# Kernel optimization log

Hardware: AMD Instinct MI355X
Metric: run time of the kernel (lower is better)

Reference implementation:

```python
import jax, jax.numpy as jnp
import numpy as np

HEADS = 8
DIM_HEAD = 64


def setup_inputs() -> dict:
    key = jax.random.key(0)
    ks = jax.random.split(key, 10)
    B, NQ, NK, D, INNER = 4, 2048, 2048, 1024, HEADS * DIM_HEAD
    w_scale = 0.02
    return {
        "x": jax.random.normal(ks[0], (B, NQ, D), jnp.float32),
        "context": jax.random.normal(ks[1], (B, NK, D), jnp.float32),
        "wq": jax.random.normal(ks[2], (D, INNER), jnp.float32) * w_scale,
        "bq": jax.random.normal(ks[3], (INNER,), jnp.float32) * w_scale,
        "wk": jax.random.normal(ks[4], (D, INNER), jnp.float32) * w_scale,
        "bk": jax.random.normal(ks[5], (INNER,), jnp.float32) * w_scale,
        "wv": jax.random.normal(ks[6], (D, INNER), jnp.float32) * w_scale,
        "bv": jax.random.normal(ks[7], (INNER,), jnp.float32) * w_scale,
        "wo": jax.random.normal(ks[8], (INNER, D), jnp.float32) * w_scale,
        "bo": jax.random.normal(ks[9], (D,), jnp.float32) * w_scale,
    }


def _split_heads(t):
    # [b, n, h*d] -> [b, h, n, d]
    b, n, _ = t.shape
    return t.reshape(b, n, HEADS, DIM_HEAD).transpose(0, 2, 1, 3)


def reference(x, context, wq, bq, wk, bk, wv, bv, wo, bo):
    scale = DIM_HEAD ** -0.5
    q = _split_heads(x @ wq + bq)        # [b, h, nq, d]
    k = _split_heads(context @ wk + bk)  # [b, h, nk, d]
    v = _split_heads(context @ wv + bv)  # [b, h, nk, d]
    sim = jnp.einsum('bhid,bhjd->bhij', q, k) * scale  # full score matrix, as in original
    attn = jax.nn.softmax(sim, axis=-1)
    out = jnp.einsum('bhij,bhjd->bhid', attn, v)       # [b, h, nq, d]
    b, h, n, d = out.shape
    out = out.transpose(0, 2, 1, 3).reshape(b, n, h * d)
    return out @ wo + bo
```

## Files before the change

### kernel.cpp

```cpp
#include <hip/hip_runtime.h>
#include <hip/hip_bf16.h>

typedef __attribute__((ext_vector_type(8))) short short8;
typedef __attribute__((ext_vector_type(4))) float f32x4;
typedef __attribute__((ext_vector_type(2))) unsigned uint2u;

__device__ __forceinline__ short f2bf(float f) {
  union { float f; unsigned u; } x; x.f = f;
  unsigned r = x.u + 0x7fffu + ((x.u >> 16) & 1u);
  return (short)(r >> 16);
}

__device__ __forceinline__ unsigned cvt_pk_bf16(float a, float b) {
  unsigned r;
  asm("v_cvt_pk_bf16_f32 %0, %1, %2" : "=v"(r) : "v"(a), "v"(b));
  return r;
}

__device__ __forceinline__ float fast_exp2(float x) {
#if __has_builtin(__builtin_amdgcn_exp2f)
  return __builtin_amdgcn_exp2f(x);
#else
  return exp2f(x);
#endif
}

__device__ __forceinline__ void gload16(const short* g, short* l) {
  __builtin_amdgcn_global_load_lds(
      (const __attribute__((address_space(1))) unsigned*)g,
      (__attribute__((address_space(3))) unsigned*)l, 16, 0, 0);
}

__device__ __forceinline__ void barrier_lgkm() {
  asm volatile("s_waitcnt lgkmcnt(0)" ::: "memory");
  __builtin_amdgcn_s_barrier();
}

__global__ __launch_bounds__(256) void prep_kernel(
    const float* __restrict__ x, const float* __restrict__ ctx,
    const float* __restrict__ wq, const float* __restrict__ wk,
    const float* __restrict__ wv, const float* __restrict__ wo,
    short* __restrict__ xc, short* __restrict__ wqt, short* __restrict__ wkt,
    short* __restrict__ wvt, short* __restrict__ wot) {
  __shared__ short tile[64][72];
  int bx = blockIdx.x;
  if (bx < 16384) {
    int i = (bx * 256 + threadIdx.x) * 4;
    const float* s = (i < (1 << 23)) ? x : ctx;
    int j = i & ((1 << 23) - 1);
    float4 f = *(const float4*)(s + j);
    union { short s[4]; uint2 u; } o;
    o.s[0] = f2bf(f.x); o.s[1] = f2bf(f.y);
    o.s[2] = f2bf(f.z); o.s[3] = f2bf(f.w);
    *(uint2*)(xc + i) = o.u;
    return;
  }
  int t = bx - 16384;
  int z = t >> 7, bb = t & 127;
  const float* src = (z == 0) ? wq : (z == 1) ? wk : (z == 2) ? wv : wo;
  short* dst = (z == 0) ? wqt : (z == 1) ? wkt : (z == 2) ? wvt : wot;
  int R = (z < 3) ? 1024 : 512, C = (z < 3) ? 512 : 1024;
  int tpc = C >> 6;
  int bxx = bb % tpc, by = bb / tpc;
  int r0 = by * 64, c0 = bxx * 64;
  int tx = threadIdx.x & 15, ty = threadIdx.x >> 4;
#pragma unroll
  for (int i = 0; i < 4; i++) {
    int r = i * 16 + ty;
    float4 f = *(const float4*)(src + (size_t)(r0 + r) * C + c0 + tx * 4);
    union { short s[4]; uint2 u; } o;
    o.s[0] = f2bf(f.x); o.s[1] = f2bf(f.y);
    o.s[2] = f2bf(f.z); o.s[3] = f2bf(f.w);
    *(uint2*)&tile[r][tx * 4] = o.u;
  }
  __syncthreads();
#pragma unroll
  for (int i = 0; i < 4; i++) {
    int c = i * 16 + ty;
    union { short s[4]; uint2 u; } o;
#pragma unroll
    for (int k = 0; k < 4; k++) o.s[k] = tile[tx * 4 + k][c];
    *(uint2*)(dst + (size_t)(c0 + c) * R + r0 + tx * 4) = o.u;
  }
}


template <bool SWAP>
__device__ __forceinline__ void gemm_core_2ph(
    const short* __restrict__ A, const short* __restrict__ Bt, int K,
    int mblk, int nblk, short* sA, short* sB, f32x4 (&acc)[4][4]) {
  int tid = threadIdx.x;
  int lane = tid & 63, wave = tid >> 6;
  int quad = lane >> 4, l15 = lane & 15;
  int wm = (wave >> 1) * 64, wn = (wave & 1) * 64;
  int sub = lane >> 3, e8 = lane & 7;
  int swz = (e8 ^ sub) << 3;
  int s0 = (quad ^ (l15 & 7)) << 3;
  const short* Ag = A + (size_t)(mblk + 32 * wave + sub) * K + swz;
  const short* Bg = Bt + (size_t)(nblk + 32 * wave + sub) * K + swz;
  short* Al = sA + 4 * wave * 512;
  short* Bl = sB + 4 * wave * 512;

  auto STAGE = [&](int b, int k0) {
    short* a = Al + b * 8192;
    short* bb = Bl + b * 8192;
#pragma unroll
    for (int t = 0; t < 4; t++) {
      gload16(Ag + (size_t)(8 * t) * K + k0, a + t * 512);
      gload16(Bg + (size_t)(8 * t) * K + k0, bb + t * 512);
    }
  };

  int nsteps = K >> 6;
  STAGE(0, 0);
  __syncthreads();
  int buf = 0;
  for (int step = 0; step < nsteps; ++step) {
    if (step + 1 < nsteps) STAGE(buf ^ 1, (step + 1) << 6);
    const short* sAb = sA + buf * 8192;
    const short* sBb = sB + buf * 8192;
#pragma unroll
    for (int h = 0; h < 2; h++) {
      int so = s0 ^ (h << 5);
      short8 af[4], bf[4];
#pragma unroll
      for (int mt = 0; mt < 4; mt++)
        af[mt] = *(const short8*)(&sAb[(wm + mt * 16 + l15) * 64 + so]);
#pragma unroll
      for (int nt = 0; nt < 4; nt++)
        bf[nt] = *(const short8*)(&sBb[(wn + nt * 16 + l15) * 64 + so]);
#pragma unroll
      for (int mt = 0; mt < 4; mt++)
#pragma unroll
        for (int nt = 0; nt < 4; nt++) {
          if (SWAP)
            acc[mt][nt] = __builtin_amdgcn_mfma_f32_16x16x32_bf16(
                bf[nt], af[mt], acc[mt][nt], 0, 0, 0);
          else
            acc[mt][nt] = __builtin_amdgcn_mfma_f32_16x16x32_bf16(
                af[mt], bf[nt], acc[mt][nt], 0, 0, 0);
        }
    }
    __syncthreads();
    buf ^= 1;
  }
}

template <bool SWAP>
__device__ __forceinline__ void gemm_core_1buf(
    const short* __restrict__ A, const short* __restrict__ Bt, int K,
    int mblk, int nblk, short* sA, short* sB, f32x4 (&acc)[4][4]) {
  int tid = threadIdx.x;
  int lane = tid & 63, wave = tid >> 6;
  int quad = lane >> 4, l15 = lane & 15;
  int wm = (wave >> 1) * 64, wn = (wave & 1) * 64;
  int sub = lane >> 3, e8 = lane & 7;
  int swz = (e8 ^ sub) << 3;
  int s0 = (quad ^ (l15 & 7)) << 3;
  const short* Ag = A + (size_t)(mblk + 32 * wave + sub) * K + swz;
  const short* Bg = Bt + (size_t)(nblk + 32 * wave + sub) * K + swz;
  short* Al = sA + 4 * wave * 512;
  short* Bl = sB + 4 * wave * 512;

  for (int k0 = 0; k0 < K; k0 += 64) {
    __syncthreads();
#pragma unroll
    for (int t = 0; t < 4; t++) {
      gload16(Ag + (size_t)(8 * t) * K + k0, Al + t * 512);
      gload16(Bg + (size_t)(8 * t) * K + k0, Bl + t * 512);
    }
    __syncthreads();
#pragma unroll
    for (int h = 0; h < 2; h++) {
      int so = s0 ^ (h << 5);
      short8 af[4], bf[4];
#pragma unroll
      for (int mt = 0; mt < 4; mt++)
        af[mt] = *(const short8*)(&sA[(wm + mt * 16 + l15) * 64 + so]);
#pragma unroll
      for (int nt = 0; nt < 4; nt++)
        bf[nt] = *(const short8*)(&sB[(wn + nt * 16 + l15) * 64 + so]);
#pragma unroll
      for (int mt = 0; mt < 4; mt++)
#pragma unroll
        for (int nt = 0; nt < 4; nt++) {
          if (SWAP)
            acc[mt][nt] = __builtin_amdgcn_mfma_f32_16x16x32_bf16(
                bf[nt], af[mt], acc[mt][nt], 0, 0, 0);
          else
            acc[mt][nt] = __builtin_amdgcn_mfma_f32_16x16x32_bf16(
                af[mt], bf[nt], acc[mt][nt], 0, 0, 0);
        }
    }
  }
}

__global__ __launch_bounds__(256) void gemm_qkv(
    const short* __restrict__ xb, const short* __restrict__ cb,
    const short* __restrict__ wqt, const short* __restrict__ wkt,
    const short* __restrict__ wvt,
    const float* __restrict__ bq, const float* __restrict__ bk,
    const float* __restrict__ bv,
    short* __restrict__ Qb, short* __restrict__ Kb, short* __restrict__ Vt) {
  __shared__ __align__(16) short sA[2 * 128 * 64];
  __shared__ __align__(16) short sB[2 * 128 * 64];
  int z = blockIdx.z;
  const short* A  = (z == 0) ? xb : cb;
  const short* Bt = (z == 0) ? wqt : (z == 1) ? wkt : wvt;
  const float* bias = (z == 0) ? bq : (z == 1) ? bk : bv;
  short* out = (z == 0) ? Qb : (z == 1) ? Kb : Vt;
  float scale = (z == 0) ? 0.18033688011112042f : 1.0f;
  int mblk = blockIdx.x * 128, nblk = blockIdx.y * 128;
  int lane = threadIdx.x & 63, wave = threadIdx.x >> 6;
  int quad = lane >> 4, l15 = lane & 15;
  int wm = (wave >> 1) * 64, wn = (wave & 1) * 64;

  if (z == 2) {
    f32x4 acc[4][4] = {};
    gemm_core_2ph<false>(A, Bt, 1024, mblk, nblk, sA, sB, acc);
#pragma unroll
    for (int nt = 0; nt < 4; nt++) {
      int col = nblk + wn + nt * 16 + l15;
      float bias_v = bias[col];
      int h = col >> 6, dh = col & 63;
#pragma unroll
      for (int mt = 0; mt < 4; mt++) {
        int row0 = mblk + wm + mt * 16 + quad * 4;
        int b = row0 >> 11, n0 = row0 & 2047;
        size_t base = ((size_t)(b * 8 + h)) << 17;
        union { short s[4]; uint2 u; } pk;
#pragma unroll
        for (int r = 0; r < 4; r++) pk.s[r] = f2bf(acc[mt][nt][r] + bias_v);
        *(uint2*)(out + base + ((size_t)dh << 11) + n0) = pk.u;
      }
    }
  } else {
    f32x4 acc[4][4] = {};
    gemm_core_2ph<true>(A, Bt, 1024, mblk, nblk, sA, sB, acc);
#pragma unroll
    for (int nt = 0; nt < 4; nt++) {
      int colbase = nblk + wn + nt * 16 + quad * 4;
      float4 b4 = *(const float4*)(bias + colbase);
      int h = colbase >> 6, dh0 = colbase & 63;
#pragma unroll
      for (int mt = 0; mt < 4; mt++) {
        int row = mblk + wm + mt * 16 + l15;
        int b = row >> 11, n = row & 2047;
        size_t base = ((size_t)(b * 8 + h)) << 17;
        union { short s[4]; uint2 u; } pk;
        pk.s[0] = f2bf((acc[mt][nt][0] + b4.x) * scale);
        pk.s[1] = f2bf((acc[mt][nt][1] + b4.y) * scale);
        pk.s[2] = f2bf((acc[mt][nt][2] + b4.z) * scale);
        pk.s[3] = f2bf((acc[mt][nt][3] + b4.w) * scale);
        *(uint2*)(out + base + ((size_t)n << 6) + dh0) = pk.u;
      }
    }
  }
}

__global__ __launch_bounds__(256) void gemm_out(
    const short* __restrict__ Ob, const short* __restrict__ wot,
    const float* __restrict__ bo, float* __restrict__ out) {
  __shared__ __align__(16) short sA[128 * 64];
  __shared__ __align__(16) short sB[128 * 64];
  int mblk = blockIdx.x * 128, nblk = blockIdx.y * 128;
  f32x4 acc[4][4] = {};
  gemm_core_1buf<true>(Ob, wot, 512, mblk, nblk, sA, sB, acc);
  int lane = threadIdx.x & 63, wave = threadIdx.x >> 6;
  int quad = lane >> 4, l15 = lane & 15;
  int wm = (wave >> 1) * 64, wn = (wave & 1) * 64;
#pragma unroll
  for (int nt = 0; nt < 4; nt++) {
    int colbase = nblk + wn + nt * 16 + quad * 4;
    float4 b4 = *(const float4*)(bo + colbase);
#pragma unroll
    for (int mt = 0; mt < 4; mt++) {
      int row = mblk + wm + mt * 16 + l15;
      f32x4 v;
      v[0] = acc[mt][nt][0] + b4.x; v[1] = acc[mt][nt][1] + b4.y;
      v[2] = acc[mt][nt][2] + b4.z; v[3] = acc[mt][nt][3] + b4.w;
      *(f32x4*)(out + (size_t)row * 1024 + colbase) = v;
    }
  }
}

__global__ __launch_bounds__(256, 2) void attn_kernel(
    const short* __restrict__ Qb, const short* __restrict__ Kb,
    const short* __restrict__ Vt, short* __restrict__ Ob) {
  __shared__ __align__(16) short sK[2 * 64 * 64];
  __shared__ __align__(16) short sV[2 * 64 * 64];
  int tid = threadIdx.x;
  int lane = tid & 63, wave = tid >> 6;
  int quad = lane >> 4, l15 = lane & 15;
  int bh = blockIdx.x & 31;
  int qt = blockIdx.x >> 5;
  const short* Qp = Qb + ((size_t)bh << 17);
  const short* Kp = Kb + ((size_t)bh << 17);
  const short* Vp = Vt + ((size_t)bh << 17);
  int qrow0 = qt * 128 + wave * 32;

  short8 qf[2][2];
#pragma unroll
  for (int g = 0; g < 2; g++) {
    const short* qrow = Qp + (size_t)(qrow0 + g * 16 + l15) * 64;
    qf[g][0] = *(const short8*)(qrow + quad * 8);
    qf[g][1] = *(const short8*)(qrow + 32 + quad * 8);
  }

  int jk0 = 2 * wave, jk1 = 2 * wave + 1;
  int sub = lane >> 3;
  int e8  = lane & 7;
  int swz = (e8 ^ sub) << 3;
  const short* kg0 = Kp + (size_t)(8 * jk0 + sub) * 64 + e8 * 8;
  const short* kg1 = Kp + (size_t)(8 * jk1 + sub) * 64 + e8 * 8;
  const short* vg0 = Vp + (size_t)(8 * jk0 + sub) * 2048 + e8 * 8;
  const short* vg1 = Vp + (size_t)(8 * jk1 + sub) * 2048 + e8 * 8;
  int kw0 = (8 * jk0 + sub) * 64 + swz;
  int kw1 = (8 * jk1 + sub) * 64 + swz;

  int s0 = (quad ^ (l15 & 7)) << 3;
  int s1 = s0 ^ 32;

  f32x4 o[2][4] = {};
  float lsum[2] = {0.f, 0.f};

  uint4 rk0 = *(const uint4*)kg0, rk1 = *(const uint4*)kg1;
  uint4 rv0 = *(const uint4*)vg0, rv1 = *(const uint4*)vg1;
  *(uint4*)(sK + kw0) = rk0; *(uint4*)(sK + kw1) = rk1;
  *(uint4*)(sV + kw0) = rv0; *(uint4*)(sV + kw1) = rv1;
  rk0 = *(const uint4*)(kg0 + 4096); rk1 = *(const uint4*)(kg1 + 4096);
  rv0 = *(const uint4*)(vg0 + 64);   rv1 = *(const uint4*)(vg1 + 64);
  barrier_lgkm();

  for (int it = 0; it < 32; ++it) {
    const short* sKr = sK + (it & 1) * 4096;
    const short* sVr = sV + (it & 1) * 4096;
    if (it < 31) {
      short* sKw = sK + ((it & 1) ^ 1) * 4096;
      short* sVw = sV + ((it & 1) ^ 1) * 4096;
      *(uint4*)(sKw + kw0) = rk0; *(uint4*)(sKw + kw1) = rk1;
      *(uint4*)(sVw + kw0) = rv0; *(uint4*)(sVw + kw1) = rv1;
      if (it < 30) {
        size_t ko = (size_t)(it + 2) * 4096;
        size_t vo = (size_t)(it + 2) * 64;
        rk0 = *(const uint4*)(kg0 + ko); rk1 = *(const uint4*)(kg1 + ko);
        rv0 = *(const uint4*)(vg0 + vo); rv1 = *(const uint4*)(vg1 + vo);
      }
    }
    unsigned xp[2][4][2];
#pragma unroll
    for (int jt = 0; jt < 4; jt++) {
      short8 k0 = *(const short8*)(&sKr[(jt * 16 + l15) * 64 + s0]);
      short8 k1 = *(const short8*)(&sKr[(jt * 16 + l15) * 64 + s1]);
#pragma unroll
      for (int g = 0; g < 2; g++) {
        f32x4 zz = {0.f, 0.f, 0.f, 0.f};
        __builtin_amdgcn_s_setprio(1);
        zz = __builtin_amdgcn_mfma_f32_16x16x32_bf16(k0, qf[g][0], zz, 0, 0, 0);
        f32x4 st = __builtin_amdgcn_mfma_f32_16x16x32_bf16(k1, qf[g][1], zz, 0, 0, 0);
        __builtin_amdgcn_s_setprio(0);
        float p0 = fast_exp2(st[0]), p1 = fast_exp2(st[1]);
        float p2 = fast_exp2(st[2]), p3 = fast_exp2(st[3]);
        lsum[g] += (p0 + p1) + (p2 + p3);
        xp[g][jt][0] = cvt_pk_bf16(p0, p1);
        xp[g][jt][1] = cvt_pk_bf16(p2, p3);
      }
    }
    short8 pf[2][2];
#pragma unroll
    for (int g = 0; g < 2; g++) {
#pragma unroll
      for (int hb = 0; hb < 2; hb++) {
        unsigned x0 = xp[g][2 * hb][0], x1 = xp[g][2 * hb][1];
        unsigned x2 = xp[g][2 * hb + 1][0], x3 = xp[g][2 * hb + 1][1];
        uint2u r1 = __builtin_amdgcn_permlane32_swap(x0, x2, false, false);
        uint2u r2 = __builtin_amdgcn_permlane16_swap(r1[0], r1[1], false, false);
        uint2u r3 = __builtin_amdgcn_permlane32_swap(x1, x3, false, false);
        uint2u r4 = __builtin_amdgcn_permlane16_swap(r3[0], r3[1], false, false);
        union { unsigned u[4]; short8 s; } P;
        P.u[0] = r2[0]; P.u[1] = r4[0]; P.u[2] = r2[1]; P.u[3] = r4[1];
        pf[g][hb] = P.s;
      }
    }
    __builtin_amdgcn_s_setprio(1);
#pragma unroll
    for (int nt = 0; nt < 4; nt++) {
      short8 v0 = *(const short8*)(&sVr[(nt * 16 + l15) * 64 + s0]);
      short8 v1 = *(const short8*)(&sVr[(nt * 16 + l15) * 64 + s1]);
#pragma unroll
      for (int g = 0; g < 2; g++) {
        o[g][nt] = __builtin_amdgcn_mfma_f32_16x16x32_bf16(v0, pf[g][0], o[g][nt], 0, 0, 0);
        o[g][nt] = __builtin_amdgcn_mfma_f32_16x16x32_bf16(v1, pf[g][1], o[g][nt], 0, 0, 0);
      }
    }
    __builtin_amdgcn_s_setprio(0);
    if (it < 31) barrier_lgkm();
  }

  int b = bh >> 3, h = bh & 7;
#pragma unroll
  for (int g = 0; g < 2; g++) {
    float l = lsum[g];
    l += __shfl_xor(l, 16, 64);
    l += __shfl_xor(l, 32, 64);
    float inv = 1.0f / l;
    size_t rowbase = ((size_t)b * 2048 + qrow0 + g * 16 + l15) * 512 + h * 64 + quad * 4;
#pragma unroll
    for (int nt = 0; nt < 4; nt++) {
      union { short s[4]; uint2 u; } pk2;
#pragma unroll
      for (int r = 0; r < 4; r++) pk2.s[r] = f2bf(o[g][nt][r] * inv);
      *(uint2*)(Ob + rowbase + nt * 16) = pk2.u;
    }
  }
}

extern "C" void kernel_launch(void* const* d_in, const int* in_sizes, int n_in,
                              void* d_out, int out_size, void* d_ws, size_t ws_size,
                              hipStream_t stream) {
  const float* x   = (const float*)d_in[0];
  const float* ctx = (const float*)d_in[1];
  const float* wq  = (const float*)d_in[2];
  const float* bq  = (const float*)d_in[3];
  const float* wk  = (const float*)d_in[4];
  const float* bk  = (const float*)d_in[5];
  const float* wv  = (const float*)d_in[6];
  const float* bv  = (const float*)d_in[7];
  const float* wo  = (const float*)d_in[8];
  const float* bo  = (const float*)d_in[9];
  float* out = (float*)d_out;
  char* ws = (char*)d_ws;

  short* xb  = (short*)(ws);
  short* cb  = (short*)(ws + (16ull << 20));
  short* wqt = (short*)(ws + (32ull << 20));
  short* wkt = (short*)(ws + (33ull << 20));
  short* wvt = (short*)(ws + (34ull << 20));
  short* wot = (short*)(ws + (35ull << 20));
  short* Qb  = (short*)(ws + (36ull << 20));
  short* Kb  = (short*)(ws + (44ull << 20));
  short* Vt  = (short*)(ws + (52ull << 20));
  short* Ob  = (short*)(ws + (60ull << 20));

  prep_kernel<<<16896, 256, 0, stream>>>(x, ctx, wq, wk, wv, wo,
                                         xb, wqt, wkt, wvt, wot);
  gemm_qkv<<<dim3(64, 4, 3), 256, 0, stream>>>(xb, cb, wqt, wkt, wvt,
                                               bq, bk, bv, Qb, Kb, Vt);
  attn_kernel<<<512, 256, 0, stream>>>(Qb, Kb, Vt, Ob);
  gemm_out<<<dim3(64, 8), 256, 0, stream>>>(Ob, wot, bo, out);
}
```

Baseline: 230.1 us.

## Split attention KV range across two wave groups and merge partial outputs in LDS

The attention block grows to 512 threads, and the two groups of four waves each handle half of the key/value sequence with their own double-buffered LDS tiles. Partial outputs and row sums from the second group go through shared memory and are added by the first group before normalisation. This halves the serial loop length per block and raises waves per CU, which should hide latency better, at the cost of doubled LDS use, an extra reduction step and possible register pressure under launch_bounds(512,4). The prep kernel is also split into separate cast and transpose launches, which adds a kernel launch.

```diff
diff --git a/kernel.cpp b/kernel.cpp
--- a/kernel.cpp
+++ b/kernel.cpp
@@ -36,33 +36,32 @@
   __builtin_amdgcn_s_barrier();
 }
 
-__global__ __launch_bounds__(256) void prep_kernel(
-    const float* __restrict__ x, const float* __restrict__ ctx,
+__global__ void cast2_bf16_kernel(const float* __restrict__ a,
+                                  const float* __restrict__ b,
+                                  short* __restrict__ dst) {
+  int i = (blockIdx.x * 256 + threadIdx.x) * 4;
+  const float* s = (i < (1 << 23)) ? a : b;
+  int j = i & ((1 << 23) - 1);
+  float4 f = *(const float4*)(s + j);
+  union { short s[4]; uint2 u; } o;
+  o.s[0] = f2bf(f.x); o.s[1] = f2bf(f.y);
+  o.s[2] = f2bf(f.z); o.s[3] = f2bf(f.w);
+  *(uint2*)(dst + i) = o.u;
+}
+
+__global__ __launch_bounds__(256) void transpose_cast4_kernel(
     const float* __restrict__ wq, const float* __restrict__ wk,
     const float* __restrict__ wv, const float* __restrict__ wo,
-    short* __restrict__ xc, short* __restrict__ wqt, short* __restrict__ wkt,
+    short* __restrict__ wqt, short* __restrict__ wkt,
     short* __restrict__ wvt, short* __restrict__ wot) {
   __shared__ short tile[64][72];
-  int bx = blockIdx.x;
-  if (bx < 16384) {
-    int i = (bx * 256 + threadIdx.x) * 4;
-    const float* s = (i < (1 << 23)) ? x : ctx;
-    int j = i & ((1 << 23) - 1);
-    float4 f = *(const float4*)(s + j);
-    union { short s[4]; uint2 u; } o;
-    o.s[0] = f2bf(f.x); o.s[1] = f2bf(f.y);
-    o.s[2] = f2bf(f.z); o.s[3] = f2bf(f.w);
-    *(uint2*)(xc + i) = o.u;
-    return;
-  }
-  int t = bx - 16384;
-  int z = t >> 7, bb = t & 127;
+  int z = blockIdx.z;
   const float* src = (z == 0) ? wq : (z == 1) ? wk : (z == 2) ? wv : wo;
   short* dst = (z == 0) ? wqt : (z == 1) ? wkt : (z == 2) ? wvt : wot;
   int R = (z < 3) ? 1024 : 512, C = (z < 3) ? 512 : 1024;
   int tpc = C >> 6;
-  int bxx = bb % tpc, by = bb / tpc;
-  int r0 = by * 64, c0 = bxx * 64;
+  int bx = blockIdx.x % tpc, by = blockIdx.x / tpc;
+  int r0 = by * 64, c0 = bx * 64;
   int tx = threadIdx.x & 15, ty = threadIdx.x >> 4;
 #pragma unroll
   for (int i = 0; i < 4; i++) {
@@ -284,20 +283,22 @@
   }
 }
 
-__global__ __launch_bounds__(256, 2) void attn_kernel(
+__global__ __launch_bounds__(512, 4) void attn_kernel(
     const short* __restrict__ Qb, const short* __restrict__ Kb,
     const short* __restrict__ Vt, short* __restrict__ Ob) {
-  __shared__ __align__(16) short sK[2 * 64 * 64];
-  __shared__ __align__(16) short sV[2 * 64 * 64];
+  __shared__ __align__(16) short sK[2 * 2 * 64 * 64];
+  __shared__ __align__(16) short sV[2 * 2 * 64 * 64];
   int tid = threadIdx.x;
   int lane = tid & 63, wave = tid >> 6;
+  int wq = wave & 3, kh = wave >> 2;
   int quad = lane >> 4, l15 = lane & 15;
   int bh = blockIdx.x & 31;
   int qt = blockIdx.x >> 5;
   const short* Qp = Qb + ((size_t)bh << 17);
   const short* Kp = Kb + ((size_t)bh << 17);
   const short* Vp = Vt + ((size_t)bh << 17);
-  int qrow0 = qt * 128 + wave * 32;
+  int qrow0 = qt * 128 + wq * 32;
+  int t0 = kh * 16;
 
   short8 qf[2][2];
 #pragma unroll
@@ -307,7 +308,7 @@
     qf[g][1] = *(const short8*)(qrow + 32 + quad * 8);
   }
 
-  int jk0 = 2 * wave, jk1 = 2 * wave + 1;
+  int jk0 = 2 * wq, jk1 = 2 * wq + 1;
   int sub = lane >> 3;
   int e8  = lane & 7;
   int swz = (e8 ^ sub) << 3;
@@ -315,6 +316,7 @@
   const short* kg1 = Kp + (size_t)(8 * jk1 + sub) * 64 + e8 * 8;
   const short* vg0 = Vp + (size_t)(8 * jk0 + sub) * 2048 + e8 * 8;
   const short* vg1 = Vp + (size_t)(8 * jk1 + sub) * 2048 + e8 * 8;
+  int kbase = kh * 8192;
   int kw0 = (8 * jk0 + sub) * 64 + swz;
   int kw1 = (8 * jk1 + sub) * 64 + swz;
 
@@ -324,25 +326,29 @@
   f32x4 o[2][4] = {};
   float lsum[2] = {0.f, 0.f};
 
-  uint4 rk0 = *(const uint4*)kg0, rk1 = *(const uint4*)kg1;
-  uint4 rv0 = *(const uint4*)vg0, rv1 = *(const uint4*)vg1;
-  *(uint4*)(sK + kw0) = rk0; *(uint4*)(sK + kw1) = rk1;
-  *(uint4*)(sV + kw0) = rv0; *(uint4*)(sV + kw1) = rv1;
-  rk0 = *(const uint4*)(kg0 + 4096); rk1 = *(const uint4*)(kg1 + 4096);
-  rv0 = *(const uint4*)(vg0 + 64);   rv1 = *(const uint4*)(vg1 + 64);
+  uint4 rk0 = *(const uint4*)(kg0 + (size_t)t0 * 4096);
+  uint4 rk1 = *(const uint4*)(kg1 + (size_t)t0 * 4096);
+  uint4 rv0 = *(const uint4*)(vg0 + (size_t)t0 * 64);
+  uint4 rv1 = *(const uint4*)(vg1 + (size_t)t0 * 64);
+  *(uint4*)(sK + kbase + kw0) = rk0; *(uint4*)(sK + kbase + kw1) = rk1;
+  *(uint4*)(sV + kbase + kw0) = rv0; *(uint4*)(sV + kbase + kw1) = rv1;
+  rk0 = *(const uint4*)(kg0 + (size_t)(t0 + 1) * 4096);
+  rk1 = *(const uint4*)(kg1 + (size_t)(t0 + 1) * 4096);
+  rv0 = *(const uint4*)(vg0 + (size_t)(t0 + 1) * 64);
+  rv1 = *(const uint4*)(vg1 + (size_t)(t0 + 1) * 64);
   barrier_lgkm();
 
-  for (int it = 0; it < 32; ++it) {
-    const short* sKr = sK + (it & 1) * 4096;
-    const short* sVr = sV + (it & 1) * 4096;
-    if (it < 31) {
-      short* sKw = sK + ((it & 1) ^ 1) * 4096;
-      short* sVw = sV + ((it & 1) ^ 1) * 4096;
+  for (int it = 0; it < 16; ++it) {
+    const short* sKr = sK + kbase + (it & 1) * 4096;
+    const short* sVr = sV + kbase + (it & 1) * 4096;
+    if (it < 15) {
+      short* sKw = sK + kbase + ((it & 1) ^ 1) * 4096;
+      short* sVw = sV + kbase + ((it & 1) ^ 1) * 4096;
       *(uint4*)(sKw + kw0) = rk0; *(uint4*)(sKw + kw1) = rk1;
       *(uint4*)(sVw + kw0) = rv0; *(uint4*)(sVw + kw1) = rv1;
-      if (it < 30) {
-        size_t ko = (size_t)(it + 2) * 4096;
-        size_t vo = (size_t)(it + 2) * 64;
+      if (it < 14) {
+        size_t ko = (size_t)(t0 + it + 2) * 4096;
+        size_t vo = (size_t)(t0 + it + 2) * 64;
         rk0 = *(const uint4*)(kg0 + ko); rk1 = *(const uint4*)(kg1 + ko);
         rv0 = *(const uint4*)(vg0 + vo); rv1 = *(const uint4*)(vg1 + vo);
       }
@@ -394,23 +400,47 @@
       }
     }
     __builtin_amdgcn_s_setprio(0);
-    if (it < 31) barrier_lgkm();
-  }
-
-  int b = bh >> 3, h = bh & 7;
+    if (it < 15) barrier_lgkm();
+  }
+
+  float lred[2];
 #pragma unroll
   for (int g = 0; g < 2; g++) {
     float l = lsum[g];
     l += __shfl_xor(l, 16, 64);
     l += __shfl_xor(l, 32, 64);
-    float inv = 1.0f / l;
-    size_t rowbase = ((size_t)b * 2048 + qrow0 + g * 16 + l15) * 512 + h * 64 + quad * 4;
-#pragma unroll
-    for (int nt = 0; nt < 4; nt++) {
-      union { short s[4]; uint2 u; } pk2;
-#pragma unroll
-      for (int r = 0; r < 4; r++) pk2.s[r] = f2bf(o[g][nt][r] * inv);
-      *(uint2*)(Ob + rowbase + nt * 16) = pk2.u;
+    lred[g] = l;
+  }
+
+  __syncthreads();
+  float* ovb = (float*)sV;
+  float* lsb = (float*)sK;
+  if (kh == 1) {
+    float* dst = ovb + wq * 2048;
+#pragma unroll
+    for (int g = 0; g < 2; g++)
+#pragma unroll
+      for (int nt = 0; nt < 4; nt++)
+        *(f32x4*)(dst + (g * 4 + nt) * 256 + lane * 4) = o[g][nt];
+    if (lane < 32) lsb[wq * 32 + lane] = lred[lane >> 4];
+  }
+  __syncthreads();
+  if (kh == 0) {
+    const float* src = ovb + wq * 2048;
+    int b = bh >> 3, h = bh & 7;
+#pragma unroll
+    for (int g = 0; g < 2; g++) {
+      float inv = 1.0f / (lred[g] + lsb[wq * 32 + g * 16 + l15]);
+      size_t rowbase = ((size_t)b * 2048 + qrow0 + g * 16 + l15) * 512 + h * 64 + quad * 4;
+#pragma unroll
+      for (int nt = 0; nt < 4; nt++) {
+        f32x4 po = *(const f32x4*)(src + (g * 4 + nt) * 256 + lane * 4);
+        union { short s[4]; uint2 u; } pk2;
+#pragma unroll
+        for (int r = 0; r < 4; r++)
+          pk2.s[r] = f2bf((o[g][nt][r] + po[r]) * inv);
+        *(uint2*)(Ob + rowbase + nt * 16) = pk2.u;
+      }
     }
   }
 }
@@ -442,10 +472,11 @@
   short* Vt  = (short*)(ws + (52ull << 20));
   short* Ob  = (short*)(ws + (60ull << 20));
 
-  prep_kernel<<<16896, 256, 0, stream>>>(x, ctx, wq, wk, wv, wo,
-                                         xb, wqt, wkt, wvt, wot);
+  cast2_bf16_kernel<<<16384, 256, 0, stream>>>(x, ctx, xb);
+  transpose_cast4_kernel<<<dim3(128, 1, 4), 256, 0, stream>>>(
+      wq, wk, wv, wo, wqt, wkt, wvt, wot);
   gemm_qkv<<<dim3(64, 4, 3), 256, 0, stream>>>(xb, cb, wqt, wkt, wvt,
                                                bq, bk, bv, Qb, Kb, Vt);
-  attn_kernel<<<512, 256, 0, stream>>>(Qb, Kb, Vt, Ob);
+  attn_kernel<<<512, 512, 0, stream>>>(Qb, Kb, Vt, Ob);
   gemm_out<<<dim3(64, 8), 256, 0, stream>>>(Ob, wot, bo, out);
 }
```

After: 246.7 us. 1.07x slower.

## Prefetch two K-steps ahead in QKV GEMM using vmcnt-counted waits

Applied to the files above, without the earlier changes.

The QKV projection GEMM loop now issues loads for the next two K tiles up front and waits with s_waitcnt vmcnt(8) plus a raw barrier instead of a full __syncthreads. Loads for tile step+2 are issued into the buffer just consumed, after a barrier. This keeps more global-to-LDS traffic in flight during the MFMA work. The combined prep kernel is also split into a separate cast kernel and a weight transpose kernel, which adds one launch. The vmcnt counts rely on each STAGE issuing exactly 8 loads per thread.

```diff
diff --git a/kernel.cpp b/kernel.cpp
--- a/kernel.cpp
+++ b/kernel.cpp
@@ -36,33 +36,32 @@
   __builtin_amdgcn_s_barrier();
 }
 
-__global__ __launch_bounds__(256) void prep_kernel(
-    const float* __restrict__ x, const float* __restrict__ ctx,
+__global__ void cast2_bf16_kernel(const float* __restrict__ a,
+                                  const float* __restrict__ b,
+                                  short* __restrict__ dst) {
+  int i = (blockIdx.x * 256 + threadIdx.x) * 4;
+  const float* s = (i < (1 << 23)) ? a : b;
+  int j = i & ((1 << 23) - 1);
+  float4 f = *(const float4*)(s + j);
+  union { short s[4]; uint2 u; } o;
+  o.s[0] = f2bf(f.x); o.s[1] = f2bf(f.y);
+  o.s[2] = f2bf(f.z); o.s[3] = f2bf(f.w);
+  *(uint2*)(dst + i) = o.u;
+}
+
+__global__ __launch_bounds__(256) void transpose_cast4_kernel(
     const float* __restrict__ wq, const float* __restrict__ wk,
     const float* __restrict__ wv, const float* __restrict__ wo,
-    short* __restrict__ xc, short* __restrict__ wqt, short* __restrict__ wkt,
+    short* __restrict__ wqt, short* __restrict__ wkt,
     short* __restrict__ wvt, short* __restrict__ wot) {
   __shared__ short tile[64][72];
-  int bx = blockIdx.x;
-  if (bx < 16384) {
-    int i = (bx * 256 + threadIdx.x) * 4;
-    const float* s = (i < (1 << 23)) ? x : ctx;
-    int j = i & ((1 << 23) - 1);
-    float4 f = *(const float4*)(s + j);
-    union { short s[4]; uint2 u; } o;
-    o.s[0] = f2bf(f.x); o.s[1] = f2bf(f.y);
-    o.s[2] = f2bf(f.z); o.s[3] = f2bf(f.w);
-    *(uint2*)(xc + i) = o.u;
-    return;
-  }
-  int t = bx - 16384;
-  int z = t >> 7, bb = t & 127;
+  int z = blockIdx.z;
   const float* src = (z == 0) ? wq : (z == 1) ? wk : (z == 2) ? wv : wo;
   short* dst = (z == 0) ? wqt : (z == 1) ? wkt : (z == 2) ? wvt : wot;
   int R = (z < 3) ? 1024 : 512, C = (z < 3) ? 512 : 1024;
   int tpc = C >> 6;
-  int bxx = bb % tpc, by = bb / tpc;
-  int r0 = by * 64, c0 = bxx * 64;
+  int bx = blockIdx.x % tpc, by = blockIdx.x / tpc;
+  int r0 = by * 64, c0 = bx * 64;
   int tx = threadIdx.x & 15, ty = threadIdx.x >> 4;
 #pragma unroll
   for (int i = 0; i < 4; i++) {
@@ -86,7 +85,7 @@
 
 
 template <bool SWAP>
-__device__ __forceinline__ void gemm_core_2ph(
+__device__ __forceinline__ void gemm_core_cnt(
     const short* __restrict__ A, const short* __restrict__ Bt, int K,
     int mblk, int nblk, short* sA, short* sB, f32x4 (&acc)[4][4]) {
   int tid = threadIdx.x;
@@ -113,12 +112,12 @@
 
   int nsteps = K >> 6;
   STAGE(0, 0);
-  __syncthreads();
-  int buf = 0;
+  STAGE(1, 1 << 6);
+  asm volatile("s_waitcnt vmcnt(8)" ::: "memory");
+  __builtin_amdgcn_s_barrier();
   for (int step = 0; step < nsteps; ++step) {
-    if (step + 1 < nsteps) STAGE(buf ^ 1, (step + 1) << 6);
-    const short* sAb = sA + buf * 8192;
-    const short* sBb = sB + buf * 8192;
+    const short* sAb = sA + (step & 1) * 8192;
+    const short* sBb = sB + (step & 1) * 8192;
 #pragma unroll
     for (int h = 0; h < 2; h++) {
       int so = s0 ^ (h << 5);
@@ -141,8 +140,16 @@
                 af[mt], bf[nt], acc[mt][nt], 0, 0, 0);
         }
     }
-    __syncthreads();
-    buf ^= 1;
+    if (step + 1 < nsteps) {
+      barrier_lgkm();
+      if (step + 2 < nsteps) {
+        STAGE(step & 1, (step + 2) << 6);
+        asm volatile("s_waitcnt vmcnt(8)" ::: "memory");
+      } else {
+        asm volatile("s_waitcnt vmcnt(0)" ::: "memory");
+      }
+      __builtin_amdgcn_s_barrier();
+    }
   }
 }
 
@@ -217,7 +224,7 @@
 
   if (z == 2) {
     f32x4 acc[4][4] = {};
-    gemm_core_2ph<false>(A, Bt, 1024, mblk, nblk, sA, sB, acc);
+    gemm_core_cnt<false>(A, Bt, 1024, mblk, nblk, sA, sB, acc);
 #pragma unroll
     for (int nt = 0; nt < 4; nt++) {
       int col = nblk + wn + nt * 16 + l15;
@@ -236,7 +243,7 @@
     }
   } else {
     f32x4 acc[4][4] = {};
-    gemm_core_2ph<true>(A, Bt, 1024, mblk, nblk, sA, sB, acc);
+    gemm_core_cnt<true>(A, Bt, 1024, mblk, nblk, sA, sB, acc);
 #pragma unroll
     for (int nt = 0; nt < 4; nt++) {
       int colbase = nblk + wn + nt * 16 + quad * 4;
@@ -442,8 +449,9 @@
   short* Vt  = (short*)(ws + (52ull << 20));
   short* Ob  = (short*)(ws + (60ull << 20));
 
-  prep_kernel<<<16896, 256, 0, stream>>>(x, ctx, wq, wk, wv, wo,
-                                         xb, wqt, wkt, wvt, wot);
+  cast2_bf16_kernel<<<16384, 256, 0, stream>>>(x, ctx, xb);
+  transpose_cast4_kernel<<<dim3(128, 1, 4), 256, 0, stream>>>(
+      wq, wk, wv, wo, wqt, wkt, wvt, wot);
   gemm_qkv<<<dim3(64, 4, 3), 256, 0, stream>>>(xb, cb, wqt, wkt, wvt,
                                                bq, bk, bv, Qb, Kb, Vt);
   attn_kernel<<<512, 256, 0, stream>>>(Qb, Kb, Vt, Ob);
```

After: 224.1 us. 2.6% less time.
